# Kernel tuning notes

Measured on AMD Instinct MI355X. Metric: run time of the kernel, lower is better.

Reference implementation:

```python
import jax, jax.numpy as jnp
import numpy as np

SMOOTH = 9.0   # self.labmda
EPS = 1e-8
MASK_VAL = -1.0

I, R, D = 64, 36, 1024   # n_image, n_regions, d
C, W = 64, 32            # n_caption, max_n_word


def setup_inputs() -> dict:
    key = jax.random.key(0)
    k1, k2, k3, k4 = jax.random.split(key, 4)
    imgs = jax.random.normal(k1, (I, R, D), dtype=jnp.float32)
    caps = jax.random.normal(k2, (C, W, D), dtype=jnp.float32)
    img_lens = jax.random.randint(k3, (I,), 1, R + 1)
    cap_lens = jnp.maximum(jax.random.randint(k4, (C,), 0, W + 1), 4)
    return {"imgs": imgs, "caps": caps, "img_lens": img_lens, "cap_lens": cap_lens}


def reference(imgs, caps, img_lens, cap_lens):
    # imgs: (I,R,D) images/regions; caps: (C,W,D); cap_lens: (C,)
    # Vectorized over captions: padded word positions are masked so the
    # per-caption word-dim l2norm matches the ragged torch loop exactly.
    wmask = jnp.arange(W)[None, :] < cap_lens[:, None]          # (C,W)
    wmask_f = wmask.astype(imgs.dtype)

    # attn[c,i,w,r] = <caps[c,w], imgs[i,r]>  (torch: bmm(context, queryT))
    attn = jnp.einsum('ird,cwd->ciwr', imgs, caps)              # (C,I,W,R)
    attn = jax.nn.leaky_relu(attn, 0.1)
    attn = attn * wmask_f[:, None, :, None]                     # zero padded words
    # l2norm over word dim (torch l2norm(attn, 2) on (I,R,W)): eps after sqrt
    norm_w = jnp.sqrt(jnp.sum(attn * attn, axis=2, keepdims=True)) + EPS
    attn = attn / norm_w
    # temperature-scaled softmax over regions
    attn = jax.nn.softmax(attn * SMOOTH, axis=3)                # (C,I,W,R)

    # weighted context per word, l2-normalized over feature dim
    wctx = jnp.einsum('ciwr,ird->ciwd', attn, imgs)             # (C,I,W,D)
    wctx = wctx / (jnp.sqrt(jnp.sum(wctx * wctx, axis=-1, keepdims=True)) + EPS)

    # cosine similarity between the word and its attended context
    cap_e = caps[:, None, :, :]                                 # (C,1,W,D)
    w12 = jnp.sum(cap_e * wctx, axis=-1)                        # (C,I,W)
    w1 = jnp.sqrt(jnp.sum(cap_e * cap_e, axis=-1))
    w2 = jnp.sqrt(jnp.sum(wctx * wctx, axis=-1))
    sim = w12 / jnp.maximum(w1 * w2, EPS)                       # (C,I,W)

    sim = jnp.where(wmask[:, None, :], sim, MASK_VAL)
    return jnp.transpose(sim, (1, 0, 2))                        # (I,C,W)
```

## Files before the change

kernel.cpp:

```cpp
#include <hip/hip_runtime.h>
#include <hip/hip_bf16.h>

#define IDIM 64
#define RDIM 36
#define DDIM 1024
#define CDIM 64
#define WDIM 32
#define SMOOTH 9.0f
#define EPSF 1e-8f

typedef __bf16 bf16_t;
typedef __bf16 bf16x8 __attribute__((ext_vector_type(8)));
typedef __bf16 bf16x4 __attribute__((ext_vector_type(4)));
typedef float f32x4 __attribute__((ext_vector_type(4)));

#define MFMA16(a, b, c) __builtin_amdgcn_mfma_f32_16x16x32_bf16((a), (b), (c), 0, 0, 0)

#define IMGSB_OFF 0
#define IMGSB_BYTES (IDIM * 4 * 12288 * 2)
#define CAPSA_OFF (IMGSB_OFF + IMGSB_BYTES)
#define CAPSA_BYTES (CDIM * 4 * 8192 * 2)
#define GRAM_OFF (CAPSA_OFF + CAPSA_BYTES)
#define GRAM_BYTES (IDIM * 48 * 48 * 4)
#define CAPN2_OFF (GRAM_OFF + GRAM_BYTES)
#define CAPN2_BYTES (CDIM * WDIM * 4)

__global__ __launch_bounds__(256, 2) void prep2(
    const float* __restrict__ imgs, const float* __restrict__ caps,
    bf16_t* __restrict__ imgsB, bf16_t* __restrict__ capsA,
    float* __restrict__ Gramf, float* __restrict__ capn2) {
  __shared__ __align__(16) char smem0[4 * 48 * 49 * 4];
  __shared__ __align__(16) bf16_t fragL[12288];
  bf16_t* ldsb = (bf16_t*)smem0;
  float (*part)[48][49] = (float(*)[48][49])smem0;

  int b = blockIdx.x, tid = threadIdx.x;
  int wv = tid >> 6, ln = tid & 63;
  int l15 = ln & 15, qd = ln >> 4;

  if (b < 256) {
    int i = b >> 2, wvk = b & 3;
    const float* src = imgs + (size_t)i * RDIM * DDIM + wvk * 256;
#pragma unroll
    for (int rep = 0; rep < 9; ++rep) {
      int idx = rep * 256 + tid;
      int row = idx >> 6, q = idx & 63;
      float4 v = *(const float4*)(src + (size_t)row * DDIM + q * 4);
      bf16x4 p;
      p[0] = (bf16_t)v.x; p[1] = (bf16_t)v.y; p[2] = (bf16_t)v.z; p[3] = (bf16_t)v.w;
      *(bf16x4*)&ldsb[row * 264 + q * 4] = p;
    }
    __syncthreads();
    bf16_t* dst = imgsB + (size_t)(i * 4 + wvk) * 12288;
#pragma unroll
    for (int rep = 0; rep < 6; ++rep) {
      int u = rep * 256 + tid;
      int kk = u / 192, rem = u - kk * 192;
      int nt = rem >> 6, lane = rem & 63, qd2 = lane >> 4, l152 = lane & 15;
      int row = nt * 16 + l152;
      bf16x8 p;
      if (row < 36) {
        p = *(const bf16x8*)&ldsb[row * 264 + kk * 32 + qd2 * 8];
      } else {
#pragma unroll
        for (int j = 0; j < 8; ++j) p[j] = (bf16_t)0.0f;
      }
      *(bf16x8*)(dst + (size_t)u * 8) = p;
      *(bf16x8*)&fragL[u * 8] = p;
    }
    __syncthreads();
    f32x4 acc[3][3];
#pragma unroll
    for (int mt = 0; mt < 3; ++mt)
#pragma unroll
      for (int nt = 0; nt < 3; ++nt) {
        f32x4 zf = {0.f, 0.f, 0.f, 0.f};
        acc[mt][nt] = zf;
      }
#pragma unroll
    for (int t = 0; t < 2; ++t) {
      int kk = wv * 2 + t;
      bf16x8 a[3];
#pragma unroll
      for (int nt = 0; nt < 3; ++nt)
        a[nt] = *(const bf16x8*)&fragL[((kk * 3 + nt) * 64 + ln) * 8];
#pragma unroll
      for (int mt = 0; mt < 3; ++mt)
#pragma unroll
        for (int nt = 0; nt < 3; ++nt)
          acc[mt][nt] = MFMA16(a[mt], a[nt], acc[mt][nt]);
    }
#pragma unroll
    for (int mt = 0; mt < 3; ++mt)
#pragma unroll
      for (int nt = 0; nt < 3; ++nt)
#pragma unroll
        for (int rg = 0; rg < 4; ++rg)
          part[wv][mt * 16 + qd * 4 + rg][nt * 16 + l15] = acc[mt][nt][rg];
    __syncthreads();
    float* gp = Gramf + (size_t)i * 2304;
#pragma unroll
    for (int it = 0; it < 9; ++it) {
      int u = it * 256 + tid;
      int r = u / 48, cc = u - r * 48;
      float v = part[0][r][cc] + part[1][r][cc] + part[2][r][cc] + part[3][r][cc];
      atomicAdd(gp + u, v);
    }
  } else {
    int bb = b - 256;
    int c = bb >> 2, wvk = bb & 3;
    const float* src = caps + (size_t)c * WDIM * DDIM + wvk * 256;
    float ss[8];
#pragma unroll
    for (int rep = 0; rep < 8; ++rep) ss[rep] = 0.f;
#pragma unroll
    for (int rep = 0; rep < 8; ++rep) {
      int idx = rep * 256 + tid;
      int row = idx >> 6, q = idx & 63;
      float4 v = *(const float4*)(src + (size_t)row * DDIM + q * 4);
      ss[rep] += v.x * v.x + v.y * v.y + v.z * v.z + v.w * v.w;
      bf16x4 p;
      p[0] = (bf16_t)v.x; p[1] = (bf16_t)v.y; p[2] = (bf16_t)v.z; p[3] = (bf16_t)v.w;
      *(bf16x4*)&ldsb[row * 264 + q * 4] = p;
    }
    __syncthreads();
    bf16_t* dst = capsA + (size_t)(c * 4 + wvk) * 8192;
#pragma unroll
    for (int rep = 0; rep < 4; ++rep) {
      int u = rep * 256 + tid;
      int kk = u >> 7, rem = u & 127;
      int mt = rem >> 6, lane = rem & 63, qd2 = lane >> 4, l152 = lane & 15;
      int row = mt * 16 + l152;
      bf16x8 p = *(const bf16x8*)&ldsb[row * 264 + kk * 32 + qd2 * 8];
      *(bf16x8*)(dst + (size_t)u * 8) = p;
    }
#pragma unroll
    for (int rep = 0; rep < 8; ++rep) {
      float s = ss[rep];
#pragma unroll
      for (int off = 32; off >= 1; off >>= 1) s += __shfl_xor(s, off, 64);
      if (ln == 0) atomicAdd(&capn2[c * 32 + rep * 4 + wv], s);
    }
  }
}

__global__ __launch_bounds__(256, 4) void main_kernel(
    const bf16_t* __restrict__ capsA, const bf16_t* __restrict__ imgsB,
    const float* __restrict__ Gramf, const float* __restrict__ capn2,
    const int* __restrict__ cap_lens, float* __restrict__ out) {
  __shared__ __align__(16) bf16_t ldsB[2][6144];

  int bx = blockIdx.x;
  int wv = threadIdx.x >> 6, ln = threadIdx.x & 63;
  int l15 = ln & 15, qd = ln >> 4;
  int xcd = bx & 7, rest = bx >> 3;
  int ih = rest & 7, cq = rest >> 3;
  int i = xcd * 8 + ih;
  int c = cq * 4 + wv;
  int clen = cap_lens[c];

  const bf16_t* Ab = capsA + (size_t)c * 32768;
  const bf16_t* Bb = imgsB + (size_t)i * 49152;

  bf16x8 t0, t1, t2;
  {
    const bf16_t* gp = Bb + wv * 1536 + ln * 8;
    t0 = *(const bf16x8*)(gp);
    t1 = *(const bf16x8*)(gp + 512);
    t2 = *(const bf16x8*)(gp + 1024);
    bf16_t* lp = &ldsB[0][wv * 1536 + ln * 8];
    *(bf16x8*)(lp) = t0;
    *(bf16x8*)(lp + 512) = t1;
    *(bf16x8*)(lp + 1024) = t2;
  }
  __syncthreads();

  f32x4 acc[2][3];
#pragma unroll
  for (int mt = 0; mt < 2; ++mt)
#pragma unroll
    for (int nt = 0; nt < 3; ++nt) {
      f32x4 zf = {0.f, 0.f, 0.f, 0.f};
      acc[mt][nt] = zf;
    }

  for (int ch = 0; ch < 8; ++ch) {
    int p = ch & 1;
    if (ch < 7) {
      const bf16_t* gp = Bb + (ch + 1) * 6144 + wv * 1536 + ln * 8;
      t0 = *(const bf16x8*)(gp);
      t1 = *(const bf16x8*)(gp + 512);
      t2 = *(const bf16x8*)(gp + 1024);
    }
#pragma unroll
    for (int j = 0; j < 4; ++j) {
      int s = ch * 4 + j;
      const bf16_t* ap = Ab + (size_t)s * 1024 + ln * 8;
      bf16x8 a0 = *(const bf16x8*)(ap);
      bf16x8 a1 = *(const bf16x8*)(ap + 512);
      const bf16_t* lp = &ldsB[p][j * 1536 + ln * 8];
      bf16x8 b0 = *(const bf16x8*)(lp);
      bf16x8 b1 = *(const bf16x8*)(lp + 512);
      bf16x8 b2 = *(const bf16x8*)(lp + 1024);
      acc[0][0] = MFMA16(a0, b0, acc[0][0]);
      acc[0][1] = MFMA16(a0, b1, acc[0][1]);
      acc[0][2] = MFMA16(a0, b2, acc[0][2]);
      acc[1][0] = MFMA16(a1, b0, acc[1][0]);
      acc[1][1] = MFMA16(a1, b1, acc[1][1]);
      acc[1][2] = MFMA16(a1, b2, acc[1][2]);
    }
    if (ch < 7) {
      bf16_t* lp = &ldsB[1 - p][wv * 1536 + ln * 8];
      *(bf16x8*)(lp) = t0;
      *(bf16x8*)(lp + 512) = t1;
      *(bf16x8*)(lp + 1024) = t2;
    }
    __syncthreads();
  }

  const float* Gb = Gramf + (size_t)i * 2304;
  bf16x8 ga[2][3];
#pragma unroll
  for (int kk = 0; kk < 2; ++kk)
#pragma unroll
    for (int nt = 0; nt < 3; ++nt) {
      bf16x8 g;
      if (kk == 1 && qd >= 2) {
#pragma unroll
        for (int j = 0; j < 8; ++j) g[j] = (bf16_t)0.0f;
      } else {
        const float* gp = Gb + (nt * 16 + l15) * 48 + kk * 32 + qd * 8;
        f32x4 u0 = *(const f32x4*)(gp);
        f32x4 u1 = *(const f32x4*)(gp + 4);
        g[0] = (bf16_t)u0[0]; g[1] = (bf16_t)u0[1];
        g[2] = (bf16_t)u0[2]; g[3] = (bf16_t)u0[3];
        g[4] = (bf16_t)u1[0]; g[5] = (bf16_t)u1[1];
        g[6] = (bf16_t)u1[2]; g[7] = (bf16_t)u1[3];
      }
      ga[kk][nt] = g;
    }

  float sinv[3];
#pragma unroll
  for (int nt = 0; nt < 3; ++nt) {
    bool padn = (nt == 2) && (l15 >= 4);
    float ns = 0.f;
#pragma unroll
    for (int mt = 0; mt < 2; ++mt)
#pragma unroll
      for (int rg = 0; rg < 4; ++rg) {
        float v = acc[mt][nt][rg];
        float l = (v > 0.f) ? v : 0.1f * v;
        int m = mt * 16 + qd * 4 + rg;
        if (m >= clen || padn) l = 0.f;
        ns += l * l;
      }
    ns += __shfl_xor(ns, 16, 64);
    ns += __shfl_xor(ns, 32, 64);
    sinv[nt] = SMOOTH / (sqrtf(ns) + EPSF);
  }

  float Srow[2][4];
#pragma unroll
  for (int mt = 0; mt < 2; ++mt)
#pragma unroll
    for (int rg = 0; rg < 4; ++rg) {
      int m = mt * 16 + qd * 4 + rg;
      bool mrow = (m >= clen);
      float z[3];
#pragma unroll
      for (int nt = 0; nt < 3; ++nt) {
        float v = acc[mt][nt][rg];
        float l = (v > 0.f) ? v : 0.1f * v;
        if (mrow) l = 0.f;
        float zz = l * sinv[nt];
        if (nt == 2 && l15 >= 4) zz = -1e30f;
        z[nt] = zz;
      }
      float mx = fmaxf(fmaxf(z[0], z[1]), z[2]);
#pragma unroll
      for (int off = 1; off < 16; off <<= 1) mx = fmaxf(mx, __shfl_xor(mx, off, 64));
      float e[3], es = 0.f;
#pragma unroll
      for (int nt = 0; nt < 3; ++nt) {
        e[nt] = __expf(z[nt] - mx);
        es += e[nt];
      }
#pragma unroll
      for (int off = 1; off < 16; off <<= 1) es += __shfl_xor(es, off, 64);
      float inv = 1.0f / es;
      float sac = 0.f;
#pragma unroll
      for (int nt = 0; nt < 3; ++nt) {
        float a = e[nt] * inv;
        sac += a * acc[mt][nt][rg];
        acc[mt][nt][rg] = a;
      }
#pragma unroll
      for (int off = 1; off < 16; off <<= 1) sac += __shfl_xor(sac, off, 64);
      Srow[mt][rg] = sac;
    }

  bf16_t* as = &ldsB[0][0] + wv * 2304;
#pragma unroll
  for (int mt = 0; mt < 2; ++mt)
#pragma unroll
    for (int nt = 0; nt < 3; ++nt)
#pragma unroll
      for (int rg = 0; rg < 4; ++rg)
        as[(mt * 16 + qd * 4 + rg) * 72 + nt * 16 + l15] = (bf16_t)acc[mt][nt][rg];
  {
    bf16x8 z8;
#pragma unroll
    for (int q = 0; q < 8; ++q) z8[q] = (bf16_t)0.0f;
    *(bf16x8*)(as + (ln >> 1) * 72 + 48 + (ln & 1) * 8) = z8;
  }
  bf16x8 fa[2][2];
#pragma unroll
  for (int mt = 0; mt < 2; ++mt)
#pragma unroll
    for (int kk = 0; kk < 2; ++kk)
      fa[mt][kk] = *(const bf16x8*)(as + (mt * 16 + l15) * 72 + kk * 32 + qd * 8);

  f32x4 y[2][3];
#pragma unroll
  for (int mt = 0; mt < 2; ++mt)
#pragma unroll
    for (int nt = 0; nt < 3; ++nt) {
      f32x4 zf = {0.f, 0.f, 0.f, 0.f};
      y[mt][nt] = zf;
    }
#pragma unroll
  for (int kk = 0; kk < 2; ++kk)
#pragma unroll
    for (int mt = 0; mt < 2; ++mt)
#pragma unroll
      for (int nt = 0; nt < 3; ++nt)
        y[mt][nt] = MFMA16(fa[mt][kk], ga[kk][nt], y[mt][nt]);

  float n2row[2][4];
#pragma unroll
  for (int mt = 0; mt < 2; ++mt)
#pragma unroll
    for (int rg = 0; rg < 4; ++rg) {
      float nn = 0.f;
#pragma unroll
      for (int nt = 0; nt < 3; ++nt) nn += y[mt][nt][rg] * acc[mt][nt][rg];
#pragma unroll
      for (int off = 1; off < 16; off <<= 1) nn += __shfl_xor(nn, off, 64);
      n2row[mt][rg] = nn;
    }

  if (l15 < 2) {
    int mt = l15;
    f32x4 cn2 = *(const f32x4*)(capn2 + c * 32 + mt * 16 + qd * 4);
    f32x4 o;
#pragma unroll
    for (int rg = 0; rg < 4; ++rg) {
      float cnv = sqrtf(cn2[rg]);
      float n2v = fmaxf(n2row[mt][rg], 0.f);
      float nrm = sqrtf(n2v);
      float den = nrm + EPSF;
      float w12 = Srow[mt][rg] / den;
      float w2 = nrm / den;
      float sim = w12 / fmaxf(cnv * w2, EPSF);
      int m = mt * 16 + qd * 4 + rg;
      if (m >= clen) sim = -1.0f;
      o[rg] = sim;
    }
    *(f32x4*)(out + ((size_t)i * CDIM + c) * WDIM + mt * 16 + qd * 4) = o;
  }
}

extern "C" void kernel_launch(void* const* d_in, const int* in_sizes, int n_in,
                              void* d_out, int out_size, void* d_ws, size_t ws_size,
                              hipStream_t stream) {
  const float* imgs = (const float*)d_in[0];
  const float* caps = (const float*)d_in[1];
  const int* cap_lens = (const int*)d_in[3];
  float* out = (float*)d_out;

  char* ws = (char*)d_ws;
  bf16_t* imgsB = (bf16_t*)(ws + IMGSB_OFF);
  bf16_t* capsA = (bf16_t*)(ws + CAPSA_OFF);
  float* Gramf = (float*)(ws + GRAM_OFF);
  float* capn2 = (float*)(ws + CAPN2_OFF);

  hipMemsetAsync(ws + GRAM_OFF, 0, GRAM_BYTES + CAPN2_BYTES, stream);
  prep2<<<512, 256, 0, stream>>>(imgs, caps, imgsB, capsA, Gramf, capn2);
  main_kernel<<<1024, 256, 0, stream>>>(capsA, imgsB, Gramf, capn2, cap_lens, out);
}
```

Baseline: 103.3 us.

## Process two images per block and replace atomics with partial-sum buffers

The main kernel now computes two images per block, so each 256-thread block reuses its caption A-fragments across twice the image work. This halves the grid and doubles the accumulator registers, and launch bounds drop to 2 blocks per SM. The prep kernel writes per-split partial Gram and caption-norm sums instead of using atomicAdd, which removes the memset launch. The consumer sums the four partials, adding extra loads in the epilogue and lowering occupancy.

```diff
diff --git a/kernel.cpp b/kernel.cpp
--- a/kernel.cpp
+++ b/kernel.cpp
@@ -20,15 +20,15 @@
 #define IMGSB_BYTES (IDIM * 4 * 12288 * 2)
 #define CAPSA_OFF (IMGSB_OFF + IMGSB_BYTES)
 #define CAPSA_BYTES (CDIM * 4 * 8192 * 2)
-#define GRAM_OFF (CAPSA_OFF + CAPSA_BYTES)
-#define GRAM_BYTES (IDIM * 48 * 48 * 4)
-#define CAPN2_OFF (GRAM_OFF + GRAM_BYTES)
-#define CAPN2_BYTES (CDIM * WDIM * 4)
+#define GPART_OFF (CAPSA_OFF + CAPSA_BYTES)
+#define GPART_BYTES (IDIM * 4 * 2304 * 4)
+#define CAPN2_OFF (GPART_OFF + GPART_BYTES)
+#define CAPN2_BYTES (CDIM * 4 * 32 * 4)
 
 __global__ __launch_bounds__(256, 2) void prep2(
     const float* __restrict__ imgs, const float* __restrict__ caps,
     bf16_t* __restrict__ imgsB, bf16_t* __restrict__ capsA,
-    float* __restrict__ Gramf, float* __restrict__ capn2) {
+    float* __restrict__ Gpart, float* __restrict__ capn2p) {
   __shared__ __align__(16) char smem0[4 * 48 * 49 * 4];
   __shared__ __align__(16) bf16_t fragL[12288];
   bf16_t* ldsb = (bf16_t*)smem0;
@@ -98,13 +98,12 @@
         for (int rg = 0; rg < 4; ++rg)
           part[wv][mt * 16 + qd * 4 + rg][nt * 16 + l15] = acc[mt][nt][rg];
     __syncthreads();
-    float* gp = Gramf + (size_t)i * 2304;
+    float* gp = Gpart + (size_t)(i * 4 + wvk) * 2304;
 #pragma unroll
     for (int it = 0; it < 9; ++it) {
       int u = it * 256 + tid;
       int r = u / 48, cc = u - r * 48;
-      float v = part[0][r][cc] + part[1][r][cc] + part[2][r][cc] + part[3][r][cc];
-      atomicAdd(gp + u, v);
+      gp[u] = part[0][r][cc] + part[1][r][cc] + part[2][r][cc] + part[3][r][cc];
     }
   } else {
     int bb = b - 256;
@@ -139,14 +138,14 @@
       float s = ss[rep];
 #pragma unroll
       for (int off = 32; off >= 1; off >>= 1) s += __shfl_xor(s, off, 64);
-      if (ln == 0) atomicAdd(&capn2[c * 32 + rep * 4 + wv], s);
+      if (ln == 0) capn2p[(c * 4 + wvk) * 32 + rep * 4 + wv] = s;
     }
   }
 }
 
-__global__ __launch_bounds__(256, 4) void main_kernel(
+__global__ __launch_bounds__(256, 2) void main_kernel(
     const bf16_t* __restrict__ capsA, const bf16_t* __restrict__ imgsB,
-    const float* __restrict__ Gramf, const float* __restrict__ capn2,
+    const float* __restrict__ Gpart, const float* __restrict__ capn2p,
     const int* __restrict__ cap_lens, float* __restrict__ out) {
   __shared__ __align__(16) bf16_t ldsB[2][6144];
 
@@ -154,20 +153,19 @@
   int wv = threadIdx.x >> 6, ln = threadIdx.x & 63;
   int l15 = ln & 15, qd = ln >> 4;
   int xcd = bx & 7, rest = bx >> 3;
-  int ih = rest & 7, cq = rest >> 3;
-  int i = xcd * 8 + ih;
+  int ip = rest & 3, cq = rest >> 2;
+  int i0 = xcd * 8 + ip * 2;
   int c = cq * 4 + wv;
   int clen = cap_lens[c];
 
   const bf16_t* Ab = capsA + (size_t)c * 32768;
-  const bf16_t* Bb = imgsB + (size_t)i * 49152;
+  const bf16_t* Bs = imgsB + (size_t)(i0 + (wv >> 1)) * 49152 + (wv & 1) * 1536 + ln * 8;
 
   bf16x8 t0, t1, t2;
   {
-    const bf16_t* gp = Bb + wv * 1536 + ln * 8;
-    t0 = *(const bf16x8*)(gp);
-    t1 = *(const bf16x8*)(gp + 512);
-    t2 = *(const bf16x8*)(gp + 1024);
+    t0 = *(const bf16x8*)(Bs);
+    t1 = *(const bf16x8*)(Bs + 512);
+    t2 = *(const bf16x8*)(Bs + 1024);
     bf16_t* lp = &ldsB[0][wv * 1536 + ln * 8];
     *(bf16x8*)(lp) = t0;
     *(bf16x8*)(lp + 512) = t1;
@@ -175,41 +173,50 @@
   }
   __syncthreads();
 
-  f32x4 acc[2][3];
+  f32x4 acc[2][6];
 #pragma unroll
   for (int mt = 0; mt < 2; ++mt)
 #pragma unroll
-    for (int nt = 0; nt < 3; ++nt) {
+    for (int nt = 0; nt < 6; ++nt) {
       f32x4 zf = {0.f, 0.f, 0.f, 0.f};
       acc[mt][nt] = zf;
     }
 
-  for (int ch = 0; ch < 8; ++ch) {
+  for (int ch = 0; ch < 16; ++ch) {
     int p = ch & 1;
-    if (ch < 7) {
-      const bf16_t* gp = Bb + (ch + 1) * 6144 + wv * 1536 + ln * 8;
+    if (ch < 15) {
+      const bf16_t* gp = Bs + (ch + 1) * 3072;
       t0 = *(const bf16x8*)(gp);
       t1 = *(const bf16x8*)(gp + 512);
       t2 = *(const bf16x8*)(gp + 1024);
     }
 #pragma unroll
-    for (int j = 0; j < 4; ++j) {
-      int s = ch * 4 + j;
+    for (int t = 0; t < 2; ++t) {
+      int s = ch * 2 + t;
       const bf16_t* ap = Ab + (size_t)s * 1024 + ln * 8;
       bf16x8 a0 = *(const bf16x8*)(ap);
       bf16x8 a1 = *(const bf16x8*)(ap + 512);
-      const bf16_t* lp = &ldsB[p][j * 1536 + ln * 8];
+      const bf16_t* lp = &ldsB[p][t * 1536 + ln * 8];
       bf16x8 b0 = *(const bf16x8*)(lp);
       bf16x8 b1 = *(const bf16x8*)(lp + 512);
       bf16x8 b2 = *(const bf16x8*)(lp + 1024);
+      bf16x8 b3 = *(const bf16x8*)(lp + 3072);
+      bf16x8 b4 = *(const bf16x8*)(lp + 3584);
+      bf16x8 b5 = *(const bf16x8*)(lp + 4096);
       acc[0][0] = MFMA16(a0, b0, acc[0][0]);
       acc[0][1] = MFMA16(a0, b1, acc[0][1]);
       acc[0][2] = MFMA16(a0, b2, acc[0][2]);
       acc[1][0] = MFMA16(a1, b0, acc[1][0]);
       acc[1][1] = MFMA16(a1, b1, acc[1][1]);
       acc[1][2] = MFMA16(a1, b2, acc[1][2]);
-    }
-    if (ch < 7) {
+      acc[0][3] = MFMA16(a0, b3, acc[0][3]);
+      acc[0][4] = MFMA16(a0, b4, acc[0][4]);
+      acc[0][5] = MFMA16(a0, b5, acc[0][5]);
+      acc[1][3] = MFMA16(a1, b3, acc[1][3]);
+      acc[1][4] = MFMA16(a1, b4, acc[1][4]);
+      acc[1][5] = MFMA16(a1, b5, acc[1][5]);
+    }
+    if (ch < 15) {
       bf16_t* lp = &ldsB[1 - p][wv * 1536 + ln * 8];
       *(bf16x8*)(lp) = t0;
       *(bf16x8*)(lp + 512) = t1;
@@ -218,157 +225,169 @@
     __syncthreads();
   }
 
-  const float* Gb = Gramf + (size_t)i * 2304;
-  bf16x8 ga[2][3];
-#pragma unroll
-  for (int kk = 0; kk < 2; ++kk)
+#pragma unroll
+  for (int ii = 0; ii < 2; ++ii) {
+    int i = i0 + ii;
+
+    const float* Gb = Gpart + (size_t)(i * 4) * 2304;
+    bf16x8 ga[2][3];
+#pragma unroll
+    for (int kk = 0; kk < 2; ++kk)
+#pragma unroll
+      for (int nt = 0; nt < 3; ++nt) {
+        bf16x8 g;
+        if (kk == 1 && qd >= 2) {
+#pragma unroll
+          for (int j = 0; j < 8; ++j) g[j] = (bf16_t)0.0f;
+        } else {
+          const float* gp = Gb + (nt * 16 + l15) * 48 + kk * 32 + qd * 8;
+          f32x4 s0 = {0.f, 0.f, 0.f, 0.f}, s1 = {0.f, 0.f, 0.f, 0.f};
+#pragma unroll
+          for (int sp = 0; sp < 4; ++sp) {
+            s0 += *(const f32x4*)(gp + sp * 2304);
+            s1 += *(const f32x4*)(gp + sp * 2304 + 4);
+          }
+          g[0] = (bf16_t)s0[0]; g[1] = (bf16_t)s0[1];
+          g[2] = (bf16_t)s0[2]; g[3] = (bf16_t)s0[3];
+          g[4] = (bf16_t)s1[0]; g[5] = (bf16_t)s1[1];
+          g[6] = (bf16_t)s1[2]; g[7] = (bf16_t)s1[3];
+        }
+        ga[kk][nt] = g;
+      }
+
+    float sinv[3];
 #pragma unroll
     for (int nt = 0; nt < 3; ++nt) {
-      bf16x8 g;
-      if (kk == 1 && qd >= 2) {
-#pragma unroll
-        for (int j = 0; j < 8; ++j) g[j] = (bf16_t)0.0f;
-      } else {
-        const float* gp = Gb + (nt * 16 + l15) * 48 + kk * 32 + qd * 8;
-        f32x4 u0 = *(const f32x4*)(gp);
-        f32x4 u1 = *(const f32x4*)(gp + 4);
-        g[0] = (bf16_t)u0[0]; g[1] = (bf16_t)u0[1];
-        g[2] = (bf16_t)u0[2]; g[3] = (bf16_t)u0[3];
-        g[4] = (bf16_t)u1[0]; g[5] = (bf16_t)u1[1];
-        g[6] = (bf16_t)u1[2]; g[7] = (bf16_t)u1[3];
-      }
-      ga[kk][nt] = g;
-    }
-
-  float sinv[3];
-#pragma unroll
-  for (int nt = 0; nt < 3; ++nt) {
-    bool padn = (nt == 2) && (l15 >= 4);
-    float ns = 0.f;
+      bool padn = (nt == 2) && (l15 >= 4);
+      float ns = 0.f;
+#pragma unroll
+      for (int mt = 0; mt < 2; ++mt)
+#pragma unroll
+        for (int rg = 0; rg < 4; ++rg) {
+          float v = acc[mt][ii * 3 + nt][rg];
+          float l = (v > 0.f) ? v : 0.1f * v;
+          int m = mt * 16 + qd * 4 + rg;
+          if (m >= clen || padn) l = 0.f;
+          ns += l * l;
+        }
+      ns += __shfl_xor(ns, 16, 64);
+      ns += __shfl_xor(ns, 32, 64);
+      sinv[nt] = SMOOTH / (sqrtf(ns) + EPSF);
+    }
+
+    float Srow[2][4];
 #pragma unroll
     for (int mt = 0; mt < 2; ++mt)
 #pragma unroll
       for (int rg = 0; rg < 4; ++rg) {
-        float v = acc[mt][nt][rg];
-        float l = (v > 0.f) ? v : 0.1f * v;
         int m = mt * 16 + qd * 4 + rg;
-        if (m >= clen || padn) l = 0.f;
-        ns += l * l;
-      }
-    ns += __shfl_xor(ns, 16, 64);
-    ns += __shfl_xor(ns, 32, 64);
-    sinv[nt] = SMOOTH / (sqrtf(ns) + EPSF);
-  }
-
-  float Srow[2][4];
-#pragma unroll
-  for (int mt = 0; mt < 2; ++mt)
-#pragma unroll
-    for (int rg = 0; rg < 4; ++rg) {
-      int m = mt * 16 + qd * 4 + rg;
-      bool mrow = (m >= clen);
-      float z[3];
+        bool mrow = (m >= clen);
+        float z[3];
+#pragma unroll
+        for (int nt = 0; nt < 3; ++nt) {
+          float v = acc[mt][ii * 3 + nt][rg];
+          float l = (v > 0.f) ? v : 0.1f * v;
+          if (mrow) l = 0.f;
+          float zz = l * sinv[nt];
+          if (nt == 2 && l15 >= 4) zz = -1e30f;
+          z[nt] = zz;
+        }
+        float mx = fmaxf(fmaxf(z[0], z[1]), z[2]);
+#pragma unroll
+        for (int off = 1; off < 16; off <<= 1) mx = fmaxf(mx, __shfl_xor(mx, off, 64));
+        float e[3], es = 0.f;
+#pragma unroll
+        for (int nt = 0; nt < 3; ++nt) {
+          e[nt] = __expf(z[nt] - mx);
+          es += e[nt];
+        }
+#pragma unroll
+        for (int off = 1; off < 16; off <<= 1) es += __shfl_xor(es, off, 64);
+        float inv = 1.0f / es;
+        float sac = 0.f;
+#pragma unroll
+        for (int nt = 0; nt < 3; ++nt) {
+          float a = e[nt] * inv;
+          sac += a * acc[mt][ii * 3 + nt][rg];
+          acc[mt][ii * 3 + nt][rg] = a;
+        }
+#pragma unroll
+        for (int off = 1; off < 16; off <<= 1) sac += __shfl_xor(sac, off, 64);
+        Srow[mt][rg] = sac;
+      }
+
+    bf16_t* as = &ldsB[0][0] + wv * 2304;
+#pragma unroll
+    for (int mt = 0; mt < 2; ++mt)
+#pragma unroll
+      for (int nt = 0; nt < 3; ++nt)
+#pragma unroll
+        for (int rg = 0; rg < 4; ++rg)
+          as[(mt * 16 + qd * 4 + rg) * 72 + nt * 16 + l15] = (bf16_t)acc[mt][ii * 3 + nt][rg];
+    {
+      bf16x8 z8;
+#pragma unroll
+      for (int q = 0; q < 8; ++q) z8[q] = (bf16_t)0.0f;
+      *(bf16x8*)(as + (ln >> 1) * 72 + 48 + (ln & 1) * 8) = z8;
+    }
+    bf16x8 fa[2][2];
+#pragma unroll
+    for (int mt = 0; mt < 2; ++mt)
+#pragma unroll
+      for (int kk = 0; kk < 2; ++kk)
+        fa[mt][kk] = *(const bf16x8*)(as + (mt * 16 + l15) * 72 + kk * 32 + qd * 8);
+
+    f32x4 y[2][3];
+#pragma unroll
+    for (int mt = 0; mt < 2; ++mt)
 #pragma unroll
       for (int nt = 0; nt < 3; ++nt) {
-        float v = acc[mt][nt][rg];
-        float l = (v > 0.f) ? v : 0.1f * v;
-        if (mrow) l = 0.f;
-        float zz = l * sinv[nt];
-        if (nt == 2 && l15 >= 4) zz = -1e30f;
-        z[nt] = zz;
-      }
-      float mx = fmaxf(fmaxf(z[0], z[1]), z[2]);
-#pragma unroll
-      for (int off = 1; off < 16; off <<= 1) mx = fmaxf(mx, __shfl_xor(mx, off, 64));
-      float e[3], es = 0.f;
-#pragma unroll
-      for (int nt = 0; nt < 3; ++nt) {
-        e[nt] = __expf(z[nt] - mx);
-        es += e[nt];
-      }
-#pragma unroll
-      for (int off = 1; off < 16; off <<= 1) es += __shfl_xor(es, off, 64);
-      float inv = 1.0f / es;
-      float sac = 0.f;
-#pragma unroll
-      for (int nt = 0; nt < 3; ++nt) {
-        float a = e[nt] * inv;
-        sac += a * acc[mt][nt][rg];
-        acc[mt][nt][rg] = a;
-      }
-#pragma unroll
-      for (int off = 1; off < 16; off <<= 1) sac += __shfl_xor(sac, off, 64);
-      Srow[mt][rg] = sac;
-    }
-
-  bf16_t* as = &ldsB[0][0] + wv * 2304;
-#pragma unroll
-  for (int mt = 0; mt < 2; ++mt)
-#pragma unroll
-    for (int nt = 0; nt < 3; ++nt)
-#pragma unroll
-      for (int rg = 0; rg < 4; ++rg)
-        as[(mt * 16 + qd * 4 + rg) * 72 + nt * 16 + l15] = (bf16_t)acc[mt][nt][rg];
-  {
-    bf16x8 z8;
-#pragma unroll
-    for (int q = 0; q < 8; ++q) z8[q] = (bf16_t)0.0f;
-    *(bf16x8*)(as + (ln >> 1) * 72 + 48 + (ln & 1) * 8) = z8;
-  }
-  bf16x8 fa[2][2];
-#pragma unroll
-  for (int mt = 0; mt < 2; ++mt)
+        f32x4 zf = {0.f, 0.f, 0.f, 0.f};
+        y[mt][nt] = zf;
+      }
 #pragma unroll
     for (int kk = 0; kk < 2; ++kk)
-      fa[mt][kk] = *(const bf16x8*)(as + (mt * 16 + l15) * 72 + kk * 32 + qd * 8);
-
-  f32x4 y[2][3];
-#pragma unroll
-  for (int mt = 0; mt < 2; ++mt)
-#pragma unroll
-    for (int nt = 0; nt < 3; ++nt) {
-      f32x4 zf = {0.f, 0.f, 0.f, 0.f};
-      y[mt][nt] = zf;
-    }
-#pragma unroll
-  for (int kk = 0; kk < 2; ++kk)
+#pragma unroll
+      for (int mt = 0; mt < 2; ++mt)
+#pragma unroll
+        for (int nt = 0; nt < 3; ++nt)
+          y[mt][nt] = MFMA16(fa[mt][kk], ga[kk][nt], y[mt][nt]);
+
+    float n2row[2][4];
 #pragma unroll
     for (int mt = 0; mt < 2; ++mt)
 #pragma unroll
-      for (int nt = 0; nt < 3; ++nt)
-        y[mt][nt] = MFMA16(fa[mt][kk], ga[kk][nt], y[mt][nt]);
-
-  float n2row[2][4];
-#pragma unroll
-  for (int mt = 0; mt < 2; ++mt)
-#pragma unroll
-    for (int rg = 0; rg < 4; ++rg) {
-      float nn = 0.f;
-#pragma unroll
-      for (int nt = 0; nt < 3; ++nt) nn += y[mt][nt][rg] * acc[mt][nt][rg];
-#pragma unroll
-      for (int off = 1; off < 16; off <<= 1) nn += __shfl_xor(nn, off, 64);
-      n2row[mt][rg] = nn;
-    }
-
-  if (l15 < 2) {
-    int mt = l15;
-    f32x4 cn2 = *(const f32x4*)(capn2 + c * 32 + mt * 16 + qd * 4);
-    f32x4 o;
-#pragma unroll
-    for (int rg = 0; rg < 4; ++rg) {
-      float cnv = sqrtf(cn2[rg]);
-      float n2v = fmaxf(n2row[mt][rg], 0.f);
-      float nrm = sqrtf(n2v);
-      float den = nrm + EPSF;
-      float w12 = Srow[mt][rg] / den;
-      float w2 = nrm / den;
-      float sim = w12 / fmaxf(cnv * w2, EPSF);
-      int m = mt * 16 + qd * 4 + rg;
-      if (m >= clen) sim = -1.0f;
-      o[rg] = sim;
-    }
-    *(f32x4*)(out + ((size_t)i * CDIM + c) * WDIM + mt * 16 + qd * 4) = o;
+      for (int rg = 0; rg < 4; ++rg) {
+        float nn = 0.f;
+#pragma unroll
+        for (int nt = 0; nt < 3; ++nt) nn += y[mt][nt][rg] * acc[mt][ii * 3 + nt][rg];
+#pragma unroll
+        for (int off = 1; off < 16; off <<= 1) nn += __shfl_xor(nn, off, 64);
+        n2row[mt][rg] = nn;
+      }
+
+    if (l15 < 2) {
+      int mt = l15;
+      f32x4 cn2 = {0.f, 0.f, 0.f, 0.f};
+#pragma unroll
+      for (int sp = 0; sp < 4; ++sp)
+        cn2 += *(const f32x4*)(capn2p + (c * 4 + sp) * 32 + mt * 16 + qd * 4);
+      f32x4 o;
+#pragma unroll
+      for (int rg = 0; rg < 4; ++rg) {
+        float cnv = sqrtf(cn2[rg]);
+        float n2v = fmaxf(n2row[mt][rg], 0.f);
+        float nrm = sqrtf(n2v);
+        float den = nrm + EPSF;
+        float w12 = Srow[mt][rg] / den;
+        float w2 = nrm / den;
+        float sim = w12 / fmaxf(cnv * w2, EPSF);
+        int m = mt * 16 + qd * 4 + rg;
+        if (m >= clen) sim = -1.0f;
+        o[rg] = sim;
+      }
+      *(f32x4*)(out + ((size_t)i * CDIM + c) * WDIM + mt * 16 + qd * 4) = o;
+    }
   }
 }
 
@@ -383,10 +402,9 @@
   char* ws = (char*)d_ws;
   bf16_t* imgsB = (bf16_t*)(ws + IMGSB_OFF);
   bf16_t* capsA = (bf16_t*)(ws + CAPSA_OFF);
-  float* Gramf = (float*)(ws + GRAM_OFF);
-  float* capn2 = (float*)(ws + CAPN2_OFF);
-
-  hipMemsetAsync(ws + GRAM_OFF, 0, GRAM_BYTES + CAPN2_BYTES, stream);
-  prep2<<<512, 256, 0, stream>>>(imgs, caps, imgsB, capsA, Gramf, capn2);
-  main_kernel<<<1024, 256, 0, stream>>>(capsA, imgsB, Gramf, capn2, cap_lens, out);
+  float* Gpart = (float*)(ws + GPART_OFF);
+  float* capn2p = (float*)(ws + CAPN2_OFF);
+
+  prep2<<<512, 256, 0, stream>>>(imgs, caps, imgsB, capsA, Gpart, capn2p);
+  main_kernel<<<512, 256, 0, stream>>>(capsA, imgsB, Gpart, capn2p, cap_lens, out);
 }
```

Result: slower. 110.4 us (+6.8%).
